# Kernel tuning notes

Measured on AMD Instinct MI355X. Metric: run time of the kernel, lower is better.

Reference implementation:

```python
import jax, jax.numpy as jnp
import numpy as np
import math

B, LQ, D = 4, 1024, 2048
H, G = 16, 4            # n_heads, n_groups
HD = D // H             # 128
GS = H // G             # group_size = 4
PAST = 1024
LK = PAST + LQ
NEG = jnp.float32(-1e30)


def _rope(x, cos, sin):
    # x: [B, L, nh, HD]; cos/sin: [1, L, 1, HD//2]; llama-style complex rotation
    x1 = x[..., 0::2]
    x2 = x[..., 1::2]
    r1 = x1 * cos - x2 * sin
    r2 = x1 * sin + x2 * cos
    return jnp.stack([r1, r2], axis=-1).reshape(x.shape)


def setup_inputs() -> dict:
    key = jax.random.key(0)
    ks = jax.random.split(key, 12)
    s = 0.02
    x = jax.random.normal(ks[0], (B, LQ, D), jnp.float32)
    past_k = jax.random.normal(ks[1], (B, G, PAST, HD), jnp.float32)
    past_v = jax.random.normal(ks[2], (B, G, PAST, HD), jnp.float32)
    rotary_freqs = jax.random.uniform(ks[3], (LQ, HD // 2), jnp.float32) * 6.283
    # causal mask with cache: query i may attend to key j if j <= PAST + i
    q_pos = PAST + jnp.arange(LQ)[:, None]
    k_pos = jnp.arange(LK)[None, :]
    mask = (k_pos <= q_pos)  # [LQ, LK] bool
    Wq = jax.random.normal(ks[4], (D, D), jnp.float32) * s
    bq = jnp.zeros((D,), jnp.float32)
    Wk = jax.random.normal(ks[5], (D, G * HD), jnp.float32) * s
    bk = jnp.zeros((G * HD,), jnp.float32)
    Wv = jax.random.normal(ks[6], (D, G * HD), jnp.float32) * s
    bv = jnp.zeros((G * HD,), jnp.float32)
    Wo = jax.random.normal(ks[7], (D, D), jnp.float32) * s
    bo = jnp.zeros((D,), jnp.float32)
    return {"x": x, "mask": mask, "rotary_freqs": rotary_freqs,
            "past_k": past_k, "past_v": past_v,
            "Wq": Wq, "bq": bq, "Wk": Wk, "bk": bk,
            "Wv": Wv, "bv": bv, "Wo": Wo, "bo": bo}


def reference(x, mask, rotary_freqs, past_k, past_v, Wq, bq, Wk, bk, Wv, bv, Wo, bo):
    # projections (torch Linear math with weights stored [in, out])
    q = (x @ Wq + bq).reshape(B, LQ, H, HD)      # break_heads: [B,L,H,HD]
    k = (x @ Wk + bk).reshape(B, LQ, G, HD)      # [B,L,G,HD]
    v = (x @ Wv + bv).reshape(B, LQ, G, HD).transpose(0, 2, 1, 3)  # [B,G,L,HD]
    # RoPE on q,k then move heads forward (matches q.transpose(2,1))
    cos = jnp.cos(rotary_freqs)[None, :, None, :]
    sin = jnp.sin(rotary_freqs)[None, :, None, :]
    q = _rope(q, cos, sin).transpose(0, 2, 1, 3)  # [B,H,LQ,HD]
    k = _rope(k, cos, sin).transpose(0, 2, 1, 3)  # [B,G,LQ,HD]
    # KV cache append
    k = jnp.concatenate([past_k, k], axis=2)      # [B,G,LK,HD]
    v = jnp.concatenate([past_v, v], axis=2)
    # grouped-query attention
    qg = q.reshape(B, G, GS, LQ, HD)
    scores = jnp.einsum('bgsqd,bgkd->bgsqk', qg, k) / math.sqrt(HD)
    scores = jnp.where(mask[None, None, None, :, :], scores, NEG)
    att = jax.nn.softmax(scores, axis=-1)
    out = jnp.einsum('bgsqk,bgkd->bgsqd', att, v).reshape(B, H, LQ, HD)
    out = out.transpose(0, 2, 1, 3).reshape(B, LQ, D)  # concatenate_heads
    return out @ Wo + bo
```

## Files before the change

### kernel.cpp

```cpp
#include <hip/hip_runtime.h>

#define B_   4
#define LQ_  1024
#define D_   2048
#define H_   16
#define G_   4
#define HD_  128
#define GS_  4
#define PAST_ 1024
#define LK_  2048
#define NQKV 3072

typedef __attribute__((ext_vector_type(8))) short short8;
typedef __attribute__((ext_vector_type(4))) float f32x4;

__device__ __forceinline__ ushort f2b(float f) {
    unsigned u = __builtin_bit_cast(unsigned, f);
    u += 0x7FFF + ((u >> 16) & 1);
    return (ushort)(u >> 16);
}
__device__ __forceinline__ float b2f(ushort h) {
    unsigned u = ((unsigned)h) << 16;
    return __builtin_bit_cast(float, u);
}

#define GLD_LDS16(gp, lp) \
    __builtin_amdgcn_global_load_lds((__attribute__((address_space(1))) void*)(gp), \
                                     (__attribute__((address_space(3))) void*)(lp), 16, 0, 0)

__global__ __launch_bounds__(256) void prep_misc(const float* __restrict__ x,
                                                 ushort* __restrict__ xb,
                                                 const float* __restrict__ pk,
                                                 ushort* __restrict__ kc,
                                                 const float* __restrict__ bq,
                                                 const float* __restrict__ bk,
                                                 const float* __restrict__ bv,
                                                 float* __restrict__ bias) {
    int blk = blockIdx.x;
    int tid = threadIdx.x;
    if (blk < 8192) {
        int i = blk * 256 + tid;
        float4 v = ((const float4*)x)[i];
        ushort4 o;
        o.x = f2b(v.x); o.y = f2b(v.y); o.z = f2b(v.z); o.w = f2b(v.w);
        ((ushort4*)xb)[i] = o;
    } else if (blk < 10240) {
        int i = (blk - 8192) * 256 + tid;
        float4 v = ((const float4*)pk)[i];
        int bg  = i >> 15;
        int rem = i & 32767;
        ushort4 o;
        o.x = f2b(v.x); o.y = f2b(v.y); o.z = f2b(v.z); o.w = f2b(v.w);
        ((ushort4*)kc)[(size_t)bg * 65536 + rem] = o;
    } else {
        int i = (blk - 10240) * 256 + tid;
        if (i < 2048) bias[i] = bq[i];
        else if (i < 2560) bias[i] = bk[i - 2048];
        else if (i < 3072) bias[i] = bv[i - 2560];
    }
}

__global__ __launch_bounds__(256) void transpose_pack(const float* __restrict__ in,
                                                      ushort* __restrict__ out,
                                                      int rows_in, int cols_in,
                                                      long in_bstride, long out_bstride,
                                                      int out_rstride) {
    __shared__ float t[32][33];
    int bz = blockIdx.z;
    in  += (long)bz * in_bstride;
    out += (long)bz * out_bstride;
    int c0 = blockIdx.x * 32, r0 = blockIdx.y * 32;
    int tx = threadIdx.x, ty = threadIdx.y;
    #pragma unroll
    for (int i = 0; i < 32; i += 8) {
        int r = r0 + ty + i;
        if (r < rows_in && (c0 + tx) < cols_in)
            t[ty + i][tx] = in[(long)r * cols_in + c0 + tx];
    }
    __syncthreads();
    #pragma unroll
    for (int i = 0; i < 32; i += 8) {
        int c = c0 + ty + i, r = r0 + tx;
        if (c < cols_in && r < rows_in)
            out[(long)c * out_rstride + r] = f2b(t[tx][ty + i]);
    }
}

__global__ __launch_bounds__(256) void vtrans(const ushort* __restrict__ qkvb,
                                              ushort* __restrict__ vtc) {
    __shared__ ushort t[64][70];
    const int bg = blockIdx.z;
    const int b = bg >> 2, g = bg & 3;
    const int d0 = blockIdx.x * 64, q0 = blockIdx.y * 64;
    const int tx = threadIdx.x, ty = threadIdx.y;
    const ushort* src = qkvb + (size_t)(b * 1024 + q0) * NQKV + 2560 + g * 128 + d0;
    #pragma unroll
    for (int i = 0; i < 64; i += 4)
        t[ty + i][tx] = src[(size_t)(ty + i) * NQKV + tx];
    __syncthreads();
    ushort* dst = vtc + ((size_t)bg * 128 + d0) * LK_ + PAST_ + q0;
    #pragma unroll
    for (int i = 0; i < 64; i += 4)
        dst[(size_t)(ty + i) * LK_ + tx] = t[tx][ty + i];
}

template <bool BF16_OUT>
__global__ __launch_bounds__(256) void gemm_bt(const ushort* __restrict__ A,
                                               const ushort* __restrict__ Bt,
                                               const float* __restrict__ bias,
                                               void* __restrict__ Cout,
                                               int M, int N, int K) {
    __shared__ ushort lA[128 * 32];
    __shared__ ushort lB[128 * 32];
    const int tid = threadIdx.x;
    const int wave = tid >> 6, lane = tid & 63;
    const int quad = lane >> 4, l15 = lane & 15;
    const int m0 = blockIdx.y * 128, n0 = blockIdx.x * 128;
    const int wm = (wave >> 1) * 64, wn = (wave & 1) * 64;

    f32x4 acc[4][4];
    #pragma unroll
    for (int i = 0; i < 4; ++i)
        #pragma unroll
        for (int j = 0; j < 4; ++j)
            #pragma unroll
            for (int r = 0; r < 4; ++r) acc[i][j][r] = 0.f;

    for (int k0 = 0; k0 < K; k0 += 32) {
        __syncthreads();
        #pragma unroll
        for (int i = 0; i < 2; ++i) {
            int chunk = wave * 2 + i;
            int flat = chunk * 512 + lane * 8;
            int row = flat >> 5, col = flat & 31;
            GLD_LDS16(A  + (size_t)(m0 + row) * K + k0 + col, lA + chunk * 512);
            GLD_LDS16(Bt + (size_t)(n0 + row) * K + k0 + col, lB + chunk * 512);
        }
        __syncthreads();
        short8 af[4], bf[4];
        #pragma unroll
        for (int i = 0; i < 4; ++i)
            af[i] = *(const short8*)(lA + (wm + i * 16 + l15) * 32 + quad * 8);
        #pragma unroll
        for (int j = 0; j < 4; ++j)
            bf[j] = *(const short8*)(lB + (wn + j * 16 + l15) * 32 + quad * 8);
        #pragma unroll
        for (int i = 0; i < 4; ++i)
            #pragma unroll
            for (int j = 0; j < 4; ++j)
                acc[i][j] = __builtin_amdgcn_mfma_f32_16x16x32_bf16(af[i], bf[j], acc[i][j], 0, 0, 0);
    }

    #pragma unroll
    for (int i = 0; i < 4; ++i)
        #pragma unroll
        for (int j = 0; j < 4; ++j)
            #pragma unroll
            for (int r = 0; r < 4; ++r) {
                int row = m0 + wm + i * 16 + quad * 4 + r;
                int col = n0 + wn + j * 16 + l15;
                float v = acc[i][j][r] + bias[col];
                if (BF16_OUT) ((ushort*)Cout)[(size_t)row * N + col] = f2b(v);
                else          ((float*)Cout)[(size_t)row * N + col] = v;
            }
}

template <bool BF16_OUT>
__global__ __launch_bounds__(512, 2) void gemm256(const ushort* __restrict__ Ap,
                                                  const ushort* __restrict__ Bp,
                                                  const float* __restrict__ bias,
                                                  void* __restrict__ Cout,
                                                  int M, int N, int K) {
    __shared__ ushort sh[65536];
    const int tid = threadIdx.x;
    const int w = tid >> 6, lane = tid & 63;
    const int quad = lane >> 4, l15 = lane & 15;
    const int wr = w >> 2, wc = w & 3;
    const int m0 = blockIdx.y * 256, n0 = blockIdx.x * 256;

    const int u0 = w * 64 + lane, u1 = (8 + w) * 64 + lane;
    const int r0_ = u0 >> 3, s0_ = u0 & 7;
    const int r1_ = u1 >> 3, s1_ = u1 & 7;
    const int sw0 = (s0_ ^ (r0_ & 7)) << 3, sw1 = (s1_ ^ (r1_ & 7)) << 3;
    const int srcA00 = (m0 + r0_) * K + sw0;
    const int srcA01 = (m0 + r1_) * K + sw1;
    const int srcA10 = (m0 + 128 + r0_) * K + sw0;
    const int srcA11 = (m0 + 128 + r1_) * K + sw1;
    const int srcB00 = (n0 + r0_) * K + sw0;
    const int srcB01 = (n0 + r1_) * K + sw1;
    const int srcB10 = (n0 + 128 + r0_) * K + sw0;
    const int srcB11 = (n0 + 128 + r1_) * K + sw1;

#define STAGE_A0(t, bufx) do { ushort* d_ = sh + (bufx) * 32768 + w * 512; \
    GLD_LDS16(Ap + (size_t)(srcA00 + (t) * 64), d_); \
    GLD_LDS16(Ap + (size_t)(srcA01 + (t) * 64), d_ + 4096); } while (0)
#define STAGE_A1(t, bufx) do { ushort* d_ = sh + (bufx) * 32768 + 8192 + w * 512; \
    GLD_LDS16(Ap + (size_t)(srcA10 + (t) * 64), d_); \
    GLD_LDS16(Ap + (size_t)(srcA11 + (t) * 64), d_ + 4096); } while (0)
#define STAGE_B0(t, bufx) do { ushort* d_ = sh + (bufx) * 32768 + 16384 + w * 512; \
    GLD_LDS16(Bp + (size_t)(srcB00 + (t) * 64), d_); \
    GLD_LDS16(Bp + (size_t)(srcB01 + (t) * 64), d_ + 4096); } while (0)
#define STAGE_B1(t, bufx) do { ushort* d_ = sh + (bufx) * 32768 + 16384 + 8192 + w * 512; \
    GLD_LDS16(Bp + (size_t)(srcB10 + (t) * 64), d_); \
    GLD_LDS16(Bp + (size_t)(srcB11 + (t) * 64), d_ + 4096); } while (0)

#define READ_A(QR) \
    _Pragma("unroll") for (int fi = 0; fi < 4; ++fi) \
    _Pragma("unroll") for (int ks = 0; ks < 2; ++ks) \
        a[fi * 2 + ks] = *(const short8*)(Ab + (wr * 128 + (QR) * 64 + fi * 16 + l15) * 64 + \
                                          (((ks * 4 + quad) ^ (l15 & 7)) << 3));
#define READ_B(QC, BREG) \
    _Pragma("unroll") for (int fj = 0; fj < 2; ++fj) \
    _Pragma("unroll") for (int ks = 0; ks < 2; ++ks) \
        BREG[fj * 2 + ks] = *(const short8*)(Bb + (wc * 64 + (QC) * 32 + fj * 16 + l15) * 64 + \
                                             (((ks * 4 + quad) ^ (l15 & 7)) << 3));
#define MFMA_Q(QR, QC, BREG) \
    _Pragma("unroll") for (int ks = 0; ks < 2; ++ks) \
    _Pragma("unroll") for (int fj = 0; fj < 2; ++fj) \
    _Pragma("unroll") for (int fi = 0; fi < 4; ++fi) \
        acc[(QR) * 4 + fi][(QC) * 2 + fj] = __builtin_amdgcn_mfma_f32_16x16x32_bf16( \
            a[fi * 2 + ks], BREG[fj * 2 + ks], acc[(QR) * 4 + fi][(QC) * 2 + fj], 0, 0, 0);

#define PH_MID() do { asm volatile("" ::: "memory"); __builtin_amdgcn_s_barrier(); \
    asm volatile("s_waitcnt lgkmcnt(0)" ::: "memory"); __builtin_amdgcn_sched_barrier(0); \
    __builtin_amdgcn_s_setprio(1); } while (0)
#define PH_END() do { __builtin_amdgcn_s_setprio(0); asm volatile("" ::: "memory"); \
    __builtin_amdgcn_s_barrier(); asm volatile("" ::: "memory"); } while (0)

    f32x4 acc[8][4];
    #pragma unroll
    for (int i = 0; i < 8; ++i)
        #pragma unroll
        for (int j = 0; j < 4; ++j)
            #pragma unroll
            for (int r = 0; r < 4; ++r) acc[i][j][r] = 0.f;

    const int KT = K >> 6;

    STAGE_A0(0, 0); STAGE_A1(0, 0); STAGE_B0(0, 0); STAGE_B1(0, 0);
    STAGE_B0(1, 1); STAGE_B1(1, 1);
    asm volatile("s_waitcnt vmcnt(4)" ::: "memory");
    asm volatile("" ::: "memory");
    __builtin_amdgcn_s_barrier();
    asm volatile("" ::: "memory");

    short8 a[8], b0[4], b1[4];
    for (int t = 0; t < KT; ++t) {
        const int buf = t & 1;
        const ushort* Ab = sh + buf * 32768;
        const ushort* Bb = Ab + 16384;

        READ_A(0)
        READ_B(0, b0)
        if (t + 1 < KT) STAGE_A0(t + 1, buf ^ 1);
        PH_MID();
        MFMA_Q(0, 0, b0)
        PH_END();

        READ_B(1, b1)
        if (t + 1 < KT) STAGE_A1(t + 1, buf ^ 1);
        PH_MID();
        MFMA_Q(0, 1, b1)
        PH_END();

        READ_A(1)
        if (t + 2 < KT) STAGE_B0(t + 2, buf);
        PH_MID();
        MFMA_Q(1, 0, b0)
        PH_END();

        if (t + 2 < KT) {
            STAGE_B1(t + 2, buf);
            asm volatile("s_waitcnt vmcnt(4)" ::: "memory");
        } else {
            asm volatile("s_waitcnt vmcnt(0)" ::: "memory");
        }
        PH_MID();
        MFMA_Q(1, 1, b1)
        PH_END();
    }

    #pragma unroll
    for (int fi = 0; fi < 8; ++fi)
        #pragma unroll
        for (int fj = 0; fj < 4; ++fj)
            #pragma unroll
            for (int r = 0; r < 4; ++r) {
                int row = m0 + wr * 128 + fi * 16 + quad * 4 + r;
                int col = n0 + wc * 64 + fj * 16 + l15;
                float v = acc[fi][fj][r] + bias[col];
                if (BF16_OUT) ((ushort*)Cout)[(size_t)row * N + col] = f2b(v);
                else          ((float*)Cout)[(size_t)row * N + col] = v;
            }
#undef STAGE_A0
#undef STAGE_A1
#undef STAGE_B0
#undef STAGE_B1
#undef READ_A
#undef READ_B
#undef MFMA_Q
#undef PH_MID
#undef PH_END
}

__global__ __launch_bounds__(256) void rope_pack(const ushort* __restrict__ qkvb,
                                                 const float* __restrict__ rf,
                                                 ushort* __restrict__ qb,
                                                 ushort* __restrict__ kc) {
    const float SC = 0.08838834764831845f;
    int row = blockIdx.x;
    int b = row >> 10, qi = row & 1023;
    int tid = threadIdx.x;
    const ushort* src = qkvb + (size_t)row * NQKV;

    for (int p = tid; p < 1024; p += 256) {
        int h = p >> 6, i = p & 63;
        float fr = rf[qi * 64 + i];
        float s, c; __sincosf(fr, &s, &c);
        uint pr = *(const uint*)(src + h * 128 + 2 * i);
        float x1 = b2f((ushort)(pr & 0xffff));
        float x2 = b2f((ushort)(pr >> 16));
        float r1 = (x1 * c - x2 * s) * SC;
        float r2 = (x1 * s + x2 * c) * SC;
        size_t o = (((size_t)(b * H_ + h)) * LQ_ + qi) * HD_ + 2 * i;
        *(uint*)(qb + o) = (uint)f2b(r1) | ((uint)f2b(r2) << 16);
    }
    {
        int g = tid >> 6, i = tid & 63;
        float fr = rf[qi * 64 + i];
        float s, c; __sincosf(fr, &s, &c);
        uint pr = *(const uint*)(src + 2048 + g * 128 + 2 * i);
        float x1 = b2f((ushort)(pr & 0xffff));
        float x2 = b2f((ushort)(pr >> 16));
        float r1 = x1 * c - x2 * s;
        float r2 = x1 * s + x2 * c;
        size_t o = (((size_t)(b * G_ + g)) * LK_ + PAST_ + qi) * HD_ + 2 * i;
        *(uint*)(kc + o) = (uint)f2b(r1) | ((uint)f2b(r2) << 16);
    }
}

__global__ __launch_bounds__(256, 2) void attn_kernel(const ushort* __restrict__ qb,
                                                      const ushort* __restrict__ kc,
                                                      const ushort* __restrict__ vtc,
                                                      ushort* __restrict__ attn_a) {
    __shared__ ushort kt[2][64 * 128];
    __shared__ ushort vtt[2][128 * 64];
    __shared__ ushort pt[128 * 64];

    const int tid = threadIdx.x;
    const int wave = tid >> 6, lane = tid & 63;
    const int quad = lane >> 4, l15 = lane & 15;
    const int qh = wave >> 1;
    const int jw = wave & 1;
    const int tile = (blockIdx.y < 32) ? blockIdx.x : (7 - (int)blockIdx.x);
    const int q0 = tile << 7;
    const int bh = blockIdx.y;
    const int b = bh >> 4, h = bh & 15, g = h >> 2;
    const ushort* kcb = kc + ((size_t)(b * G_ + g)) * LK_ * HD_;
    const ushort* vcb = vtc + ((size_t)(b * G_ + g)) * HD_ * LK_;

    int ksrc[4], vsrc[4];
    #pragma unroll
    for (int i = 0; i < 4; ++i) {
        int u = (wave * 4 + i) * 64 + lane;
        int key = u >> 4, cs = u & 15;
        ksrc[i] = key * HD_ + ((cs ^ (key & 15)) << 3);
        int d = u >> 3, c2 = u & 7;
        vsrc[i] = d * LK_ + ((c2 ^ (d & 7)) << 3);
    }

    short8 qf[4][4];
    #pragma unroll
    for (int qfr = 0; qfr < 4; ++qfr) {
        int qrow = q0 + qh * 64 + qfr * 16 + l15;
        const ushort* qp = qb + (((size_t)(b * H_ + h)) * LQ_ + qrow) * HD_ + quad * 8;
        #pragma unroll
        for (int kk = 0; kk < 4; ++kk) qf[qfr][kk] = *(const short8*)(qp + kk * 32);
    }

    f32x4 o[4][4];
    #pragma unroll
    for (int qfr = 0; qfr < 4; ++qfr)
        #pragma unroll
        for (int f = 0; f < 4; ++f)
            #pragma unroll
            for (int r = 0; r < 4; ++r) o[qfr][f][r] = 0.f;
    float lstq[4];
    #pragma unroll
    for (int qfr = 0; qfr < 4; ++qfr) lstq[qfr] = 0.f;

    const int nsteps = (PAST_ + q0 + 128) >> 6;

    #pragma unroll
    for (int i = 0; i < 4; ++i) {
        int ci = wave * 4 + i;
        GLD_LDS16(kcb + ksrc[i], kt[0] + ci * 512);
        GLD_LDS16(vcb + vsrc[i], vtt[0] + ci * 512);
    }

    for (int it = 0; it < nsteps; ++it) {
        const int k0 = it << 6;
        const int cur = it & 1, nxt = cur ^ 1;
        __syncthreads();
        if (it + 1 < nsteps) {
            const int k1 = k0 + 64;
            #pragma unroll
            for (int i = 0; i < 4; ++i) {
                int ci = wave * 4 + i;
                GLD_LDS16(kcb + (size_t)k1 * HD_ + ksrc[i], kt[nxt] + ci * 512);
                GLD_LDS16(vcb + k1 + vsrc[i], vtt[nxt] + ci * 512);
            }
        }

        f32x4 z[4][2];
        #pragma unroll
        for (int qfr = 0; qfr < 4; ++qfr)
            #pragma unroll
            for (int kf = 0; kf < 2; ++kf)
                #pragma unroll
                for (int r = 0; r < 4; ++r) z[qfr][kf][r] = 0.f;
        __builtin_amdgcn_s_setprio(1);
        #pragma unroll
        for (int kk = 0; kk < 4; ++kk) {
            #pragma unroll
            for (int kf = 0; kf < 2; ++kf) {
                int key = jw * 32 + kf * 16 + l15;
                const short8 bk = *(const short8*)(kt[cur] + key * 128 + (((kk * 4 + quad) ^ l15) << 3));
                #pragma unroll
                for (int qfr = 0; qfr < 4; ++qfr)
                    z[qfr][kf] = __builtin_amdgcn_mfma_f32_16x16x32_bf16(bk, qf[qfr][kk], z[qfr][kf], 0, 0, 0);
            }
        }
        __builtin_amdgcn_s_setprio(0);

        const bool mask_step = (it >= nsteps - 2);
        #pragma unroll
        for (int qfr = 0; qfr < 4; ++qfr) {
            const int row = qh * 64 + qfr * 16 + l15;
            #pragma unroll
            for (int kf = 0; kf < 2; ++kf) {
                float pv0[4];
                #pragma unroll
                for (int r = 0; r < 4; ++r) {
                    float pv_ = __expf(z[qfr][kf][r]);
                    if (mask_step) {
                        int keyg = k0 + jw * 32 + kf * 16 + quad * 4 + r;
                        if (keyg > PAST_ + q0 + row) pv_ = 0.f;
                    }
                    lstq[qfr] += pv_;
                    pv0[r] = pv_;
                }
                uint2 val;
                val.x = (uint)f2b(pv0[0]) | ((uint)f2b(pv0[1]) << 16);
                val.y = (uint)f2b(pv0[2]) | ((uint)f2b(pv0[3]) << 16);
                int unit = jw * 4 + kf * 2 + (quad >> 1);
                int swz = ((unit ^ (row & 7)) << 3) + ((quad & 1) << 2);
                *(uint2*)(pt + row * 64 + swz) = val;
            }
        }

        asm volatile("s_waitcnt lgkmcnt(0)" ::: "memory");
        __builtin_amdgcn_s_barrier();
        __builtin_amdgcn_sched_barrier(0);

        __builtin_amdgcn_s_setprio(1);
        #pragma unroll
        for (int j2 = 0; j2 < 2; ++j2) {
            short8 pa[4];
            #pragma unroll
            for (int qfr = 0; qfr < 4; ++qfr) {
                int prow = qh * 64 + qfr * 16 + l15;
                pa[qfr] = *(const short8*)(pt + prow * 64 + (((j2 * 4 + quad) ^ (prow & 7)) << 3));
            }
            #pragma unroll
            for (int f = 0; f < 4; ++f) {
                int d = jw * 64 + f * 16 + l15;
                const short8 bv = *(const short8*)(vtt[cur] + d * 64 + (((j2 * 4 + quad) ^ (l15 & 7)) << 3));
                #pragma unroll
                for (int qfr = 0; qfr < 4; ++qfr)
                    o[qfr][f] = __builtin_amdgcn_mfma_f32_16x16x32_bf16(pa[qfr], bv, o[qfr][f], 0, 0, 0);
            }
        }
        __builtin_amdgcn_s_setprio(0);
    }

    float rq[4];
    #pragma unroll
    for (int qfr = 0; qfr < 4; ++qfr) {
        float rs = lstq[qfr];
        rs += __shfl_xor(rs, 16);
        rs += __shfl_xor(rs, 32);
        rq[qfr] = rs;
    }
    __syncthreads();
    float* scr = (float*)pt;
    #pragma unroll
    for (int qfr = 0; qfr < 4; ++qfr)
        scr[wave * 256 + qfr * 64 + lane] = rq[qfr];
    __syncthreads();
    #pragma unroll
    for (int qfr = 0; qfr < 4; ++qfr) {
        float tot = rq[qfr] + scr[(wave ^ 1) * 256 + qfr * 64 + lane];
        float linv[4];
        #pragma unroll
        for (int r = 0; r < 4; ++r)
            linv[r] = 1.0f / __shfl(tot, quad * 4 + r, 16);
        #pragma unroll
        for (int f = 0; f < 4; ++f)
            #pragma unroll
            for (int r = 0; r < 4; ++r) {
                int q = q0 + qh * 64 + qfr * 16 + quad * 4 + r;
                int d = jw * 64 + f * 16 + l15;
                attn_a[((size_t)(b * LQ_ + q)) * D_ + h * HD_ + d] = f2b(o[qfr][f][r] * linv[r]);
            }
    }
}


extern "C" void kernel_launch(void* const* d_in, const int* in_sizes, int n_in,
                              void* d_out, int out_size, void* d_ws, size_t ws_size,
                              hipStream_t stream) {
    const float* x  = (const float*)d_in[0];
    const float* rf = (const float*)d_in[2];
    const float* pk = (const float*)d_in[3];
    const float* pv = (const float*)d_in[4];
    const float* Wq = (const float*)d_in[5];
    const float* bq = (const float*)d_in[6];
    const float* Wk = (const float*)d_in[7];
    const float* bk = (const float*)d_in[8];
    const float* Wv = (const float*)d_in[9];
    const float* bv = (const float*)d_in[10];
    const float* Wo = (const float*)d_in[11];
    const float* bo = (const float*)d_in[12];
    float* out = (float*)d_out;

    char* p = (char*)d_ws;
    auto take = [&](size_t n) { void* r = p; p += (n + 255) & ~(size_t)255; return r; };
    ushort* xb       = (ushort*)take((size_t)4096 * 2048 * 2);
    ushort* wt_qkv   = (ushort*)take((size_t)3072 * 2048 * 2);
    ushort* wt_o     = (ushort*)take((size_t)2048 * 2048 * 2);
    float*  bias_qkv = (float*) take((size_t)3072 * 4);
    ushort* qkvb     = (ushort*)take((size_t)4096 * 3072 * 2);
    ushort* qb       = (ushort*)take((size_t)B_ * H_ * LQ_ * HD_ * 2);
    ushort* kcache   = (ushort*)take((size_t)B_ * G_ * LK_ * HD_ * 2);
    ushort* vtc      = (ushort*)take((size_t)B_ * G_ * HD_ * LK_ * 2);
    ushort* attn_a   = (ushort*)take((size_t)4096 * 2048 * 2);

    dim3 tb(32, 8);
    prep_misc<<<10252, 256, 0, stream>>>(x, xb, pk, kcache, bq, bk, bv, bias_qkv);
    transpose_pack<<<dim3(64, 64, 1), tb, 0, stream>>>(Wq, wt_qkv, 2048, 2048, 0, 0, 2048);
    transpose_pack<<<dim3(16, 64, 1), tb, 0, stream>>>(Wk, wt_qkv + (size_t)2048 * 2048, 2048, 512, 0, 0, 2048);
    transpose_pack<<<dim3(16, 64, 1), tb, 0, stream>>>(Wv, wt_qkv + (size_t)2560 * 2048, 2048, 512, 0, 0, 2048);
    transpose_pack<<<dim3(64, 64, 1), tb, 0, stream>>>(Wo, wt_o, 2048, 2048, 0, 0, 2048);
    transpose_pack<<<dim3(4, 32, 16), tb, 0, stream>>>(pv, vtc, 1024, 128,
                                                       (long)1024 * 128, (long)128 * 2048, 2048);

    gemm256<true><<<dim3(12, 16), 512, 0, stream>>>(xb, wt_qkv, bias_qkv, qkvb, 4096, 3072, 2048);
    rope_pack<<<4096, 256, 0, stream>>>(qkvb, rf, qb, kcache);
    vtrans<<<dim3(2, 16, 16), dim3(64, 4), 0, stream>>>(qkvb, vtc);
    attn_kernel<<<dim3(8, 64), 256, 0, stream>>>(qb, kcache, vtc, attn_a);
    gemm_bt<false><<<dim3(16, 32), 256, 0, stream>>>(attn_a, wt_o, bo, out, 4096, 2048, 2048);
}
```

Before: 378.3 us.

## Keep softmax probabilities in registers via lane shuffles, split PV over keys

The attention kernel no longer writes the bf16 probability tile to LDS and rereads it after a barrier. Each wave builds its MFMA A operand with cross-lane shuffles and a packed bf16 convert, then multiplies against all 128 V columns for its own 32-key half. The two key-half waves' partial outputs are summed through LDS at the end. This removes one barrier and the P-tile LDS traffic per step, at the cost of twice as many output accumulators per wave (more register pressure at 2 waves/SIMD) and a final reduction pass.

```diff
diff --git a/kernel.cpp b/kernel.cpp
--- a/kernel.cpp
+++ b/kernel.cpp
@@ -13,6 +13,7 @@
 
 typedef __attribute__((ext_vector_type(8))) short short8;
 typedef __attribute__((ext_vector_type(4))) float f32x4;
+typedef __attribute__((ext_vector_type(4))) unsigned int uint4v;
 
 __device__ __forceinline__ ushort f2b(float f) {
     unsigned u = __builtin_bit_cast(unsigned, f);
@@ -22,6 +23,11 @@
 __device__ __forceinline__ float b2f(ushort h) {
     unsigned u = ((unsigned)h) << 16;
     return __builtin_bit_cast(float, u);
+}
+__device__ __forceinline__ uint pk2(float lo, float hi) {
+    uint r;
+    asm("v_cvt_pk_bf16_f32 %0, %1, %2" : "=v"(r) : "v"(lo), "v"(hi));
+    return r;
 }
 
 #define GLD_LDS16(gp, lp) \
@@ -343,9 +349,7 @@
                                                       const ushort* __restrict__ kc,
                                                       const ushort* __restrict__ vtc,
                                                       ushort* __restrict__ attn_a) {
-    __shared__ ushort kt[2][64 * 128];
-    __shared__ ushort vtt[2][128 * 64];
-    __shared__ ushort pt[128 * 64];
+    __shared__ ushort smem[36864];
 
     const int tid = threadIdx.x;
     const int wave = tid >> 6, lane = tid & 63;
@@ -378,11 +382,11 @@
         for (int kk = 0; kk < 4; ++kk) qf[qfr][kk] = *(const short8*)(qp + kk * 32);
     }
 
-    f32x4 o[4][4];
+    f32x4 o[4][8];
     #pragma unroll
     for (int qfr = 0; qfr < 4; ++qfr)
         #pragma unroll
-        for (int f = 0; f < 4; ++f)
+        for (int f = 0; f < 8; ++f)
             #pragma unroll
             for (int r = 0; r < 4; ++r) o[qfr][f][r] = 0.f;
     float lstq[4];
@@ -390,25 +394,29 @@
     for (int qfr = 0; qfr < 4; ++qfr) lstq[qfr] = 0.f;
 
     const int nsteps = (PAST_ + q0 + 128) >> 6;
+    const int srcA = ((quad & 1) << 5) + l15;
+    const bool kf_hi = (quad >= 2);
 
     #pragma unroll
     for (int i = 0; i < 4; ++i) {
         int ci = wave * 4 + i;
-        GLD_LDS16(kcb + ksrc[i], kt[0] + ci * 512);
-        GLD_LDS16(vcb + vsrc[i], vtt[0] + ci * 512);
+        GLD_LDS16(kcb + ksrc[i], smem + ci * 512);
+        GLD_LDS16(vcb + vsrc[i], smem + 16384 + ci * 512);
     }
 
     for (int it = 0; it < nsteps; ++it) {
         const int k0 = it << 6;
         const int cur = it & 1, nxt = cur ^ 1;
+        const ushort* ktc = smem + cur * 8192;
+        const ushort* vtb = smem + 16384 + cur * 8192;
         __syncthreads();
         if (it + 1 < nsteps) {
             const int k1 = k0 + 64;
             #pragma unroll
             for (int i = 0; i < 4; ++i) {
                 int ci = wave * 4 + i;
-                GLD_LDS16(kcb + (size_t)k1 * HD_ + ksrc[i], kt[nxt] + ci * 512);
-                GLD_LDS16(vcb + k1 + vsrc[i], vtt[nxt] + ci * 512);
+                GLD_LDS16(kcb + (size_t)k1 * HD_ + ksrc[i], smem + nxt * 8192 + ci * 512);
+                GLD_LDS16(vcb + k1 + vsrc[i], smem + 16384 + nxt * 8192 + ci * 512);
             }
         }
 
@@ -425,7 +433,7 @@
             #pragma unroll
             for (int kf = 0; kf < 2; ++kf) {
                 int key = jw * 32 + kf * 16 + l15;
-                const short8 bk = *(const short8*)(kt[cur] + key * 128 + (((kk * 4 + quad) ^ l15) << 3));
+                const short8 bk = *(const short8*)(ktc + key * 128 + (((kk * 4 + quad) ^ l15) << 3));
                 #pragma unroll
                 for (int qfr = 0; qfr < 4; ++qfr)
                     z[qfr][kf] = __builtin_amdgcn_mfma_f32_16x16x32_bf16(bk, qf[qfr][kk], z[qfr][kf], 0, 0, 0);
@@ -434,52 +442,42 @@
         __builtin_amdgcn_s_setprio(0);
 
         const bool mask_step = (it >= nsteps - 2);
+        short8 pa[4];
         #pragma unroll
         for (int qfr = 0; qfr < 4; ++qfr) {
-            const int row = qh * 64 + qfr * 16 + l15;
-            #pragma unroll
-            for (int kf = 0; kf < 2; ++kf) {
-                float pv0[4];
+            float p[2][4];
+            #pragma unroll
+            for (int kf = 0; kf < 2; ++kf)
                 #pragma unroll
                 for (int r = 0; r < 4; ++r) {
                     float pv_ = __expf(z[qfr][kf][r]);
                     if (mask_step) {
                         int keyg = k0 + jw * 32 + kf * 16 + quad * 4 + r;
-                        if (keyg > PAST_ + q0 + row) pv_ = 0.f;
+                        if (keyg > PAST_ + q0 + qh * 64 + qfr * 16 + l15) pv_ = 0.f;
                     }
                     lstq[qfr] += pv_;
-                    pv0[r] = pv_;
+                    p[kf][r] = pv_;
                 }
-                uint2 val;
-                val.x = (uint)f2b(pv0[0]) | ((uint)f2b(pv0[1]) << 16);
-                val.y = (uint)f2b(pv0[2]) | ((uint)f2b(pv0[3]) << 16);
-                int unit = jw * 4 + kf * 2 + (quad >> 1);
-                int swz = ((unit ^ (row & 7)) << 3) + ((quad & 1) << 2);
-                *(uint2*)(pt + row * 64 + swz) = val;
-            }
-        }
-
-        asm volatile("s_waitcnt lgkmcnt(0)" ::: "memory");
-        __builtin_amdgcn_s_barrier();
-        __builtin_amdgcn_sched_barrier(0);
+            uint lo0 = pk2(p[0][0], p[0][1]), hi0 = pk2(p[0][2], p[0][3]);
+            uint lo1 = pk2(p[1][0], p[1][1]), hi1 = pk2(p[1][2], p[1][3]);
+            uint a_lo0 = __shfl(lo0, srcA),      a_lo1 = __shfl(lo1, srcA);
+            uint a_hi0 = __shfl(hi0, srcA),      a_hi1 = __shfl(hi1, srcA);
+            uint b_lo0 = __shfl(lo0, srcA + 16), b_lo1 = __shfl(lo1, srcA + 16);
+            uint b_hi0 = __shfl(hi0, srcA + 16), b_hi1 = __shfl(hi1, srcA + 16);
+            union { uint4v u; short8 s; } cv;
+            cv.u = (uint4v){kf_hi ? a_lo1 : a_lo0, kf_hi ? a_hi1 : a_hi0,
+                            kf_hi ? b_lo1 : b_lo0, kf_hi ? b_hi1 : b_hi0};
+            pa[qfr] = cv.s;
+        }
 
         __builtin_amdgcn_s_setprio(1);
         #pragma unroll
-        for (int j2 = 0; j2 < 2; ++j2) {
-            short8 pa[4];
-            #pragma unroll
-            for (int qfr = 0; qfr < 4; ++qfr) {
-                int prow = qh * 64 + qfr * 16 + l15;
-                pa[qfr] = *(const short8*)(pt + prow * 64 + (((j2 * 4 + quad) ^ (prow & 7)) << 3));
-            }
-            #pragma unroll
-            for (int f = 0; f < 4; ++f) {
-                int d = jw * 64 + f * 16 + l15;
-                const short8 bv = *(const short8*)(vtt[cur] + d * 64 + (((j2 * 4 + quad) ^ (l15 & 7)) << 3));
-                #pragma unroll
-                for (int qfr = 0; qfr < 4; ++qfr)
-                    o[qfr][f] = __builtin_amdgcn_mfma_f32_16x16x32_bf16(pa[qfr], bv, o[qfr][f], 0, 0, 0);
-            }
+        for (int f = 0; f < 8; ++f) {
+            int d = f * 16 + l15;
+            const short8 bv = *(const short8*)(vtb + d * 64 + (((jw * 4 + quad) ^ (l15 & 7)) << 3));
+            #pragma unroll
+            for (int qfr = 0; qfr < 4; ++qfr)
+                o[qfr][f] = __builtin_amdgcn_mfma_f32_16x16x32_bf16(pa[qfr], bv, o[qfr][f], 0, 0, 0);
         }
         __builtin_amdgcn_s_setprio(0);
     }
@@ -493,26 +491,38 @@
         rq[qfr] = rs;
     }
     __syncthreads();
-    float* scr = (float*)pt;
-    #pragma unroll
-    for (int qfr = 0; qfr < 4; ++qfr)
-        scr[wave * 256 + qfr * 64 + lane] = rq[qfr];
+    float* oscr = (float*)smem;
+    float* lscr = (float*)(smem + 32768);
+    if (jw == 1) {
+        #pragma unroll
+        for (int qfr = 0; qfr < 4; ++qfr) {
+            lscr[qh * 256 + qfr * 64 + lane] = rq[qfr];
+            #pragma unroll
+            for (int f = 0; f < 8; ++f)
+                *(f32x4*)(oscr + qh * 8192 + (qfr * 8 + f) * 256 + lane * 4) = o[qfr][f];
+        }
+    }
     __syncthreads();
-    #pragma unroll
-    for (int qfr = 0; qfr < 4; ++qfr) {
-        float tot = rq[qfr] + scr[(wave ^ 1) * 256 + qfr * 64 + lane];
-        float linv[4];
-        #pragma unroll
-        for (int r = 0; r < 4; ++r)
-            linv[r] = 1.0f / __shfl(tot, quad * 4 + r, 16);
-        #pragma unroll
-        for (int f = 0; f < 4; ++f)
-            #pragma unroll
-            for (int r = 0; r < 4; ++r) {
-                int q = q0 + qh * 64 + qfr * 16 + quad * 4 + r;
-                int d = jw * 64 + f * 16 + l15;
-                attn_a[((size_t)(b * LQ_ + q)) * D_ + h * HD_ + d] = f2b(o[qfr][f][r] * linv[r]);
+    if (jw == 0) {
+        #pragma unroll
+        for (int qfr = 0; qfr < 4; ++qfr) {
+            float tot = rq[qfr] + lscr[qh * 256 + qfr * 64 + lane];
+            float linv[4];
+            #pragma unroll
+            for (int r = 0; r < 4; ++r)
+                linv[r] = 1.0f / __shfl(tot, quad * 4 + r, 16);
+            #pragma unroll
+            for (int f = 0; f < 8; ++f) {
+                f32x4 t = *(const f32x4*)(oscr + qh * 8192 + (qfr * 8 + f) * 256 + lane * 4);
+                #pragma unroll
+                for (int r = 0; r < 4; ++r) {
+                    int q = q0 + qh * 64 + qfr * 16 + quad * 4 + r;
+                    int d = f * 16 + l15;
+                    attn_a[((size_t)(b * LQ_ + q)) * D_ + h * HD_ + d] =
+                        f2b((o[qfr][f][r] + t[r]) * linv[r]);
+                }
             }
+        }
     }
 }
 
```

Measured after the change: 422.0 us. 1.12x slower.

## Replace output GEMM with pipelined 128x256 tile kernel and merge weight transposes

Applied to the files above, without the earlier changes.

Swaps the simple single-buffered 128x128 output projection GEMM for a 128x256-tile, 512-thread kernel. The new kernel uses double-buffered swizzled LDS, direct global-to-LDS loads issued ahead of use, and phased barriers with priority hints. The aim is to hide memory latency behind MFMA work and avoid LDS bank conflicts. It also merges four weight-transpose launches into one kernel to cut launch overhead, at the cost of more complex synchronization and fewer blocks (256) for the output GEMM.

```diff
diff --git a/kernel.cpp b/kernel.cpp
--- a/kernel.cpp
+++ b/kernel.cpp
@@ -60,6 +60,30 @@
     }
 }
 
+__global__ __launch_bounds__(256) void wtrans_all(const float* __restrict__ Wq,
+                                                  const float* __restrict__ Wk,
+                                                  const float* __restrict__ Wv,
+                                                  const float* __restrict__ Wo,
+                                                  ushort* __restrict__ wt_qkv,
+                                                  ushort* __restrict__ wt_o) {
+    __shared__ float t[32][33];
+    int blk = blockIdx.x;
+    const float* in; ushort* out; int cols, bx, by;
+    if (blk < 4096)      { in = Wq; out = wt_qkv;                        cols = 2048; bx = blk & 63; by = blk >> 6; }
+    else if (blk < 5120) { int i = blk - 4096; in = Wk; out = wt_qkv + (size_t)2048 * 2048; cols = 512; bx = i & 15; by = i >> 4; }
+    else if (blk < 6144) { int i = blk - 5120; in = Wv; out = wt_qkv + (size_t)2560 * 2048; cols = 512; bx = i & 15; by = i >> 4; }
+    else                 { int i = blk - 6144; in = Wo; out = wt_o;      cols = 2048; bx = i & 63; by = i >> 6; }
+    int c0 = bx * 32, r0 = by * 32;
+    int tx = threadIdx.x, ty = threadIdx.y;
+    #pragma unroll
+    for (int i = 0; i < 32; i += 8)
+        t[ty + i][tx] = in[(long)(r0 + ty + i) * cols + c0 + tx];
+    __syncthreads();
+    #pragma unroll
+    for (int i = 0; i < 32; i += 8)
+        out[(long)(c0 + ty + i) * 2048 + r0 + tx] = f2b(t[tx][ty + i]);
+}
+
 __global__ __launch_bounds__(256) void transpose_pack(const float* __restrict__ in,
                                                       ushort* __restrict__ out,
                                                       int rows_in, int cols_in,
@@ -102,67 +126,6 @@
     #pragma unroll
     for (int i = 0; i < 64; i += 4)
         dst[(size_t)(ty + i) * LK_ + tx] = t[tx][ty + i];
-}
-
-template <bool BF16_OUT>
-__global__ __launch_bounds__(256) void gemm_bt(const ushort* __restrict__ A,
-                                               const ushort* __restrict__ Bt,
-                                               const float* __restrict__ bias,
-                                               void* __restrict__ Cout,
-                                               int M, int N, int K) {
-    __shared__ ushort lA[128 * 32];
-    __shared__ ushort lB[128 * 32];
-    const int tid = threadIdx.x;
-    const int wave = tid >> 6, lane = tid & 63;
-    const int quad = lane >> 4, l15 = lane & 15;
-    const int m0 = blockIdx.y * 128, n0 = blockIdx.x * 128;
-    const int wm = (wave >> 1) * 64, wn = (wave & 1) * 64;
-
-    f32x4 acc[4][4];
-    #pragma unroll
-    for (int i = 0; i < 4; ++i)
-        #pragma unroll
-        for (int j = 0; j < 4; ++j)
-            #pragma unroll
-            for (int r = 0; r < 4; ++r) acc[i][j][r] = 0.f;
-
-    for (int k0 = 0; k0 < K; k0 += 32) {
-        __syncthreads();
-        #pragma unroll
-        for (int i = 0; i < 2; ++i) {
-            int chunk = wave * 2 + i;
-            int flat = chunk * 512 + lane * 8;
-            int row = flat >> 5, col = flat & 31;
-            GLD_LDS16(A  + (size_t)(m0 + row) * K + k0 + col, lA + chunk * 512);
-            GLD_LDS16(Bt + (size_t)(n0 + row) * K + k0 + col, lB + chunk * 512);
-        }
-        __syncthreads();
-        short8 af[4], bf[4];
-        #pragma unroll
-        for (int i = 0; i < 4; ++i)
-            af[i] = *(const short8*)(lA + (wm + i * 16 + l15) * 32 + quad * 8);
-        #pragma unroll
-        for (int j = 0; j < 4; ++j)
-            bf[j] = *(const short8*)(lB + (wn + j * 16 + l15) * 32 + quad * 8);
-        #pragma unroll
-        for (int i = 0; i < 4; ++i)
-            #pragma unroll
-            for (int j = 0; j < 4; ++j)
-                acc[i][j] = __builtin_amdgcn_mfma_f32_16x16x32_bf16(af[i], bf[j], acc[i][j], 0, 0, 0);
-    }
-
-    #pragma unroll
-    for (int i = 0; i < 4; ++i)
-        #pragma unroll
-        for (int j = 0; j < 4; ++j)
-            #pragma unroll
-            for (int r = 0; r < 4; ++r) {
-                int row = m0 + wm + i * 16 + quad * 4 + r;
-                int col = n0 + wn + j * 16 + l15;
-                float v = acc[i][j][r] + bias[col];
-                if (BF16_OUT) ((ushort*)Cout)[(size_t)row * N + col] = f2b(v);
-                else          ((float*)Cout)[(size_t)row * N + col] = v;
-            }
 }
 
 template <bool BF16_OUT>
@@ -299,6 +262,140 @@
 #undef READ_A
 #undef READ_B
 #undef MFMA_Q
+#undef PH_MID
+#undef PH_END
+}
+
+template <bool BF16_OUT>
+__global__ __launch_bounds__(512, 2) void gemm_128x256(const ushort* __restrict__ Ap,
+                                                       const ushort* __restrict__ Bp,
+                                                       const float* __restrict__ bias,
+                                                       void* __restrict__ Cout,
+                                                       int M, int N, int K) {
+    __shared__ ushort sh[49152];
+    const int tid = threadIdx.x;
+    const int w = tid >> 6, lane = tid & 63;
+    const int quad = lane >> 4, l15 = lane & 15;
+    const int wr = w >> 2, wc = w & 3;
+    const int m0 = blockIdx.y * 128, n0 = blockIdx.x * 256;
+
+    const int u0 = w * 64 + lane, u1 = (8 + w) * 64 + lane;
+    const int r0_ = u0 >> 3, s0_ = u0 & 7;
+    const int r1_ = u1 >> 3, s1_ = u1 & 7;
+    const int sw0 = (s0_ ^ (r0_ & 7)) << 3, sw1 = (s1_ ^ (r1_ & 7)) << 3;
+    const int srcA0  = (m0 + r0_) * K + sw0;
+    const int srcA1  = (m0 + 64 + r0_) * K + sw0;
+    const int srcB00 = (n0 + r0_) * K + sw0;
+    const int srcB01 = (n0 + r1_) * K + sw1;
+    const int srcB10 = (n0 + 128 + r0_) * K + sw0;
+    const int srcB11 = (n0 + 128 + r1_) * K + sw1;
+
+#define STG_A0(t, bufx) do { ushort* d_ = sh + (bufx) * 24576 + w * 512; \
+    GLD_LDS16(Ap + (size_t)(srcA0 + (t) * 64), d_); } while (0)
+#define STG_A1(t, bufx) do { ushort* d_ = sh + (bufx) * 24576 + 4096 + w * 512; \
+    GLD_LDS16(Ap + (size_t)(srcA1 + (t) * 64), d_); } while (0)
+#define STG_B0(t, bufx) do { ushort* d_ = sh + (bufx) * 24576 + 8192 + w * 512; \
+    GLD_LDS16(Bp + (size_t)(srcB00 + (t) * 64), d_); \
+    GLD_LDS16(Bp + (size_t)(srcB01 + (t) * 64), d_ + 4096); } while (0)
+#define STG_B1(t, bufx) do { ushort* d_ = sh + (bufx) * 24576 + 16384 + w * 512; \
+    GLD_LDS16(Bp + (size_t)(srcB10 + (t) * 64), d_); \
+    GLD_LDS16(Bp + (size_t)(srcB11 + (t) * 64), d_ + 4096); } while (0)
+
+#define RD_A(QR) \
+    _Pragma("unroll") for (int fi = 0; fi < 2; ++fi) \
+    _Pragma("unroll") for (int ks = 0; ks < 2; ++ks) \
+        a[fi * 2 + ks] = *(const short8*)(Ab + (wr * 64 + (QR) * 32 + fi * 16 + l15) * 64 + \
+                                          (((ks * 4 + quad) ^ (l15 & 7)) << 3));
+#define RD_B(QC, BREG) \
+    _Pragma("unroll") for (int fj = 0; fj < 2; ++fj) \
+    _Pragma("unroll") for (int ks = 0; ks < 2; ++ks) \
+        BREG[fj * 2 + ks] = *(const short8*)(Bb + (wc * 64 + (QC) * 32 + fj * 16 + l15) * 64 + \
+                                             (((ks * 4 + quad) ^ (l15 & 7)) << 3));
+#define MM_Q(QR, QC, BREG) \
+    _Pragma("unroll") for (int ks = 0; ks < 2; ++ks) \
+    _Pragma("unroll") for (int fj = 0; fj < 2; ++fj) \
+    _Pragma("unroll") for (int fi = 0; fi < 2; ++fi) \
+        acc[(QR) * 2 + fi][(QC) * 2 + fj] = __builtin_amdgcn_mfma_f32_16x16x32_bf16( \
+            a[fi * 2 + ks], BREG[fj * 2 + ks], acc[(QR) * 2 + fi][(QC) * 2 + fj], 0, 0, 0);
+
+#define PH_MID() do { asm volatile("" ::: "memory"); __builtin_amdgcn_s_barrier(); \
+    asm volatile("s_waitcnt lgkmcnt(0)" ::: "memory"); __builtin_amdgcn_sched_barrier(0); \
+    __builtin_amdgcn_s_setprio(1); } while (0)
+#define PH_END() do { __builtin_amdgcn_s_setprio(0); asm volatile("" ::: "memory"); \
+    __builtin_amdgcn_s_barrier(); asm volatile("" ::: "memory"); } while (0)
+
+    f32x4 acc[4][4];
+    #pragma unroll
+    for (int i = 0; i < 4; ++i)
+        #pragma unroll
+        for (int j = 0; j < 4; ++j)
+            #pragma unroll
+            for (int r = 0; r < 4; ++r) acc[i][j][r] = 0.f;
+
+    const int KT = K >> 6;
+
+    STG_A0(0, 0); STG_A1(0, 0); STG_B0(0, 0); STG_B1(0, 0);
+    STG_B0(1, 1); STG_B1(1, 1);
+    asm volatile("s_waitcnt vmcnt(4)" ::: "memory");
+    asm volatile("" ::: "memory");
+    __builtin_amdgcn_s_barrier();
+    asm volatile("" ::: "memory");
+
+    short8 a[4], b0[4], b1[4];
+    for (int t = 0; t < KT; ++t) {
+        const int buf = t & 1;
+        const ushort* Ab = sh + buf * 24576;
+        const ushort* Bb = Ab + 8192;
+
+        RD_A(0)
+        RD_B(0, b0)
+        if (t + 1 < KT) STG_A0(t + 1, buf ^ 1);
+        PH_MID();
+        MM_Q(0, 0, b0)
+        PH_END();
+
+        RD_B(1, b1)
+        if (t + 1 < KT) STG_A1(t + 1, buf ^ 1);
+        PH_MID();
+        MM_Q(0, 1, b1)
+        PH_END();
+
+        RD_A(1)
+        if (t + 2 < KT) STG_B0(t + 2, buf);
+        PH_MID();
+        MM_Q(1, 0, b0)
+        PH_END();
+
+        if (t + 2 < KT) {
+            STG_B1(t + 2, buf);
+            asm volatile("s_waitcnt vmcnt(4)" ::: "memory");
+        } else {
+            asm volatile("s_waitcnt vmcnt(0)" ::: "memory");
+        }
+        PH_MID();
+        MM_Q(1, 1, b1)
+        PH_END();
+    }
+
+    #pragma unroll
+    for (int fi = 0; fi < 4; ++fi)
+        #pragma unroll
+        for (int fj = 0; fj < 4; ++fj)
+            #pragma unroll
+            for (int r = 0; r < 4; ++r) {
+                int row = m0 + wr * 64 + fi * 16 + quad * 4 + r;
+                int col = n0 + wc * 64 + fj * 16 + l15;
+                float v = acc[fi][fj][r] + bias[col];
+                if (BF16_OUT) ((ushort*)Cout)[(size_t)row * N + col] = f2b(v);
+                else          ((float*)Cout)[(size_t)row * N + col] = v;
+            }
+#undef STG_A0
+#undef STG_A1
+#undef STG_B0
+#undef STG_B1
+#undef RD_A
+#undef RD_B
+#undef MM_Q
 #undef PH_MID
 #undef PH_END
 }
@@ -546,18 +643,14 @@
     ushort* vtc      = (ushort*)take((size_t)B_ * G_ * HD_ * LK_ * 2);
     ushort* attn_a   = (ushort*)take((size_t)4096 * 2048 * 2);
 
-    dim3 tb(32, 8);
     prep_misc<<<10252, 256, 0, stream>>>(x, xb, pk, kcache, bq, bk, bv, bias_qkv);
-    transpose_pack<<<dim3(64, 64, 1), tb, 0, stream>>>(Wq, wt_qkv, 2048, 2048, 0, 0, 2048);
-    transpose_pack<<<dim3(16, 64, 1), tb, 0, stream>>>(Wk, wt_qkv + (size_t)2048 * 2048, 2048, 512, 0, 0, 2048);
-    transpose_pack<<<dim3(16, 64, 1), tb, 0, stream>>>(Wv, wt_qkv + (size_t)2560 * 2048, 2048, 512, 0, 0, 2048);
-    transpose_pack<<<dim3(64, 64, 1), tb, 0, stream>>>(Wo, wt_o, 2048, 2048, 0, 0, 2048);
-    transpose_pack<<<dim3(4, 32, 16), tb, 0, stream>>>(pv, vtc, 1024, 128,
-                                                       (long)1024 * 128, (long)128 * 2048, 2048);
+    wtrans_all<<<10240, dim3(32, 8), 0, stream>>>(Wq, Wk, Wv, Wo, wt_qkv, wt_o);
+    transpose_pack<<<dim3(4, 32, 16), dim3(32, 8), 0, stream>>>(pv, vtc, 1024, 128,
+                                                                (long)1024 * 128, (long)128 * 2048, 2048);
 
     gemm256<true><<<dim3(12, 16), 512, 0, stream>>>(xb, wt_qkv, bias_qkv, qkvb, 4096, 3072, 2048);
     rope_pack<<<4096, 256, 0, stream>>>(qkvb, rf, qb, kcache);
     vtrans<<<dim3(2, 16, 16), dim3(64, 4), 0, stream>>>(qkvb, vtc);
     attn_kernel<<<dim3(8, 64), 256, 0, stream>>>(qb, kcache, vtc, attn_a);
-    gemm_bt<false><<<dim3(16, 32), 256, 0, stream>>>(attn_a, wt_o, bo, out, 4096, 2048, 2048);
-}
+    gemm_128x256<false><<<dim3(8, 32), 512, 0, stream>>>(attn_a, wt_o, bo, out, 4096, 2048, 2048);
+}
```

New measurement: 354.3 us. 1.07x faster.
